# Kernel tuning notes

Hardware: AMD Instinct MI355X
Metric: run time of the kernel (lower is better)

## Reference

```python
import jax, jax.numpy as jnp
import numpy as np

B, C, N = 64, 512, 512  # batch, channels (=in_dim), last dim (=in_dim)
OUT = 512
GROUPS = 32
EPS = 1e-5


def setup_inputs() -> dict:
    key = jax.random.key(0)
    ks = jax.random.split(key, 7)
    s = 1.0 / np.sqrt(C)
    return {
        "x": jax.random.normal(ks[0], (B, C, N), dtype=jnp.float32),
        "q_w": jax.random.normal(ks[1], (OUT, C), dtype=jnp.float32) * s,
        "q_b": jax.random.normal(ks[2], (OUT,), dtype=jnp.float32) * s,
        "k_w": jax.random.normal(ks[3], (OUT, C), dtype=jnp.float32) * s,
        "k_b": jax.random.normal(ks[4], (OUT,), dtype=jnp.float32) * s,
        "v_w": jax.random.normal(ks[5], (OUT, C), dtype=jnp.float32) * s,
        "v_b": jax.random.normal(ks[6], (OUT,), dtype=jnp.float32) * s,
        "gn_w": jnp.ones((C,), dtype=jnp.float32),
        "gn_b": jnp.zeros((C,), dtype=jnp.float32),
    }


def group_norm(x, w, b):
    # x: (B, C, N); 32 groups over channel dim, affine per-channel.
    Bb, Cc, Nn = x.shape
    xg = x.reshape(Bb, GROUPS, -1)
    mean = jnp.mean(xg, axis=-1, keepdims=True)
    var = jnp.var(xg, axis=-1, keepdims=True)
    xn = ((xg - mean) * jax.lax.rsqrt(var + EPS)).reshape(Bb, Cc, Nn)
    return xn * w[None, :, None] + b[None, :, None]


def reference(x, q_w, q_b, k_w, k_b, v_w, v_b, gn_w, gn_b):
    xn = group_norm(x, gn_w, gn_b)  # (B, C, N)
    # nn.Linear applies to the last dim (N == in_dim)
    q = jnp.einsum("bcn,dn->bcd", xn, q_w) + q_b  # (B, C, OUT)
    k = jnp.einsum("bcn,dn->bcd", xn, k_w) + k_b
    v = jnp.einsum("bcn,dn->bcd", xn, v_w) + v_b
    scale = 1.0 / jnp.sqrt(jnp.float32(OUT))
    scores = jnp.einsum("bqd,bkd->bqk", q, k) * scale  # (B, C, C)
    attn = jax.nn.softmax(scores, axis=-1)
    return jnp.einsum("bqk,bkd->bqd", attn, v)  # (B, C, OUT)
```

## Files before the change

### kernel.cpp

```cpp
#include <hip/hip_runtime.h>
#include <cstdint>

#define EPSV 1e-5f
#define SM_SCALE 0.044194173824159216f

typedef unsigned short u16;
typedef __attribute__((ext_vector_type(8))) short short8;
typedef __attribute__((ext_vector_type(4))) float f32x4;

__device__ __forceinline__ u16 f2bf(float f) {
  union { float f; uint32_t u; } v; v.f = f;
  return (u16)((v.u + 0x7FFFu + ((v.u >> 16) & 1u)) >> 16);
}

__device__ __forceinline__ float bf2f(u16 h) {
  union { uint32_t u; float f; } v; v.u = ((uint32_t)h) << 16; return v.f;
}

__device__ __forceinline__ void gload_lds16(const void* g, void* l) {
  __builtin_amdgcn_global_load_lds((const __attribute__((address_space(1))) void*)g,
                                   (__attribute__((address_space(3))) void*)l, 16, 0, 0);
}

__device__ __forceinline__ f32x4 mfma16(short8 a, short8 b, f32x4 c) {
  return __builtin_amdgcn_mfma_f32_16x16x32_bf16(a, b, c, 0, 0, 0);
}

__global__ __launch_bounds__(256) void gn_fused_k(const float* __restrict__ x,
                                                  const float* __restrict__ gw,
                                                  const float* __restrict__ gb,
                                                  u16* __restrict__ xn) {
  __shared__ float xs[8192];
  __shared__ float ls[4], lss[4];
  const int bg = blockIdx.x;
  const int g = bg & 31;
  const float* p = x + (size_t)bg * 8192;
  float s = 0.f, ss = 0.f;
#pragma unroll
  for (int i = 0; i < 8; ++i) {
    const int idx = i * 1024 + threadIdx.x * 4;
    float4 v = *reinterpret_cast<const float4*>(p + idx);
    *reinterpret_cast<float4*>(xs + idx) = v;
    s += v.x + v.y + v.z + v.w;
    ss += v.x * v.x + v.y * v.y + v.z * v.z + v.w * v.w;
  }
  for (int off = 32; off; off >>= 1) { s += __shfl_xor(s, off); ss += __shfl_xor(ss, off); }
  const int w = threadIdx.x >> 6;
  if ((threadIdx.x & 63) == 0) { ls[w] = s; lss[w] = ss; }
  __syncthreads();
  s = ls[0] + ls[1] + ls[2] + ls[3];
  ss = lss[0] + lss[1] + lss[2] + lss[3];
  const float inv_n = 1.0f / 8192.f;
  const float mean = s * inv_n;
  const float rstd = rsqrtf(ss * inv_n - mean * mean + EPSV);
#pragma unroll
  for (int j = 0; j < 4; ++j) {
    const int idx = j * 2048 + threadIdx.x * 8;
    const int c = g * 16 + (idx >> 9);
    const float sc = gw[c] * rstd;
    const float sh = gb[c] - mean * sc;
    u16 o[8];
#pragma unroll
    for (int e = 0; e < 8; ++e) o[e] = f2bf(xs[idx + e] * sc + sh);
    *reinterpret_cast<uint4*>(xn + (size_t)bg * 8192 + idx) = *reinterpret_cast<const uint4*>(o);
  }
}

__global__ __launch_bounds__(256) void cast3_k(const float* __restrict__ a,
                                               const float* __restrict__ b2,
                                               const float* __restrict__ c,
                                               u16* __restrict__ oa, u16* __restrict__ ob,
                                               u16* __restrict__ oc) {
  const int which = blockIdx.x >> 7;
  const float* in = which == 0 ? a : (which == 1 ? b2 : c);
  u16* out = which == 0 ? oa : (which == 1 ? ob : oc);
  size_t base = (((size_t)(blockIdx.x & 127)) * 256 + threadIdx.x) * 8;
  float4 v0 = *reinterpret_cast<const float4*>(in + base);
  float4 v1 = *reinterpret_cast<const float4*>(in + base + 4);
  u16 o[8];
  o[0] = f2bf(v0.x); o[1] = f2bf(v0.y); o[2] = f2bf(v0.z); o[3] = f2bf(v0.w);
  o[4] = f2bf(v1.x); o[5] = f2bf(v1.y); o[6] = f2bf(v1.z); o[7] = f2bf(v1.w);
  *reinterpret_cast<uint4*>(out + base) = *reinterpret_cast<const uint4*>(o);
}

template <int OUT_MODE>
__global__ __launch_bounds__(512, 1) void gemm256_k(const u16* __restrict__ A, size_t sA,
                                                    const u16* __restrict__ Bm, size_t sB,
                                                    const float* __restrict__ bias,
                                                    void* __restrict__ out, size_t sO) {
  __shared__ u16 smem[65536];
  const int d = blockIdx.x;
  const int wgid = (d & 7) * 32 + (d >> 3);
  const int b = wgid >> 2;
  const int tile = wgid & 3;
  const int tm = (tile >> 1) * 256, tn = (tile & 1) * 256;
  const u16* Ab = A + (size_t)b * sA;
  const u16* Bb = Bm + (size_t)b * sB;
  const int tid = threadIdx.x, w = tid >> 6, lane = tid & 63;
  const int rh = w >> 2, cw = w & 3;
  const int frow = lane & 15, cc = lane >> 4;
  f32x4 acc[8][4] = {};
  short8 af[8], bfr[2];

#define STAGEH(Lofs, Gp)                                                       \
  {                                                                            \
    const u16* gsrc_ = (Gp);                                                   \
    _Pragma("unroll")                                                          \
    for (int p_ = 0; p_ < 2; ++p_) {                                           \
      const int row_ = p_ * 64 + (tid >> 3);                                   \
      const int slot_ = (tid & 7) ^ (row_ & 7);                                \
      gload_lds16(gsrc_ + (size_t)row_ * 512 + slot_ * 8,                      \
                  &smem[(Lofs) + p_ * 4096 + tid * 8]);                        \
    }                                                                          \
  }

#define PHASE(VMN, QB, KS, CP, ...)                                            \
  {                                                                            \
    asm volatile("s_waitcnt vmcnt(" #VMN ")" ::: "memory");                    \
    __builtin_amdgcn_s_barrier();                                              \
    asm volatile("" ::: "memory");                                             \
    _Pragma("unroll")                                                          \
    for (int j_ = 0; j_ < 2; ++j_) {                                           \
      const int lrb_ = (cw & 1) * 64 + (CP) * 32 + j_ * 16 + frow;             \
      bfr[j_] = *reinterpret_cast<const short8*>(                              \
          &smem[(QB) + 16384 + (cw >> 1) * 8192 + lrb_ * 64 +                  \
                (((KS) * 4 + cc) ^ (lrb_ & 7)) * 8]);                          \
    }                                                                          \
    if ((CP) == 0) {                                                           \
      _Pragma("unroll")                                                        \
      for (int ri_ = 0; ri_ < 8; ++ri_) {                                      \
        const int lra_ = ri_ * 16 + frow;                                      \
        af[ri_] = *reinterpret_cast<const short8*>(                            \
            &smem[(QB) + rh * 8192 + lra_ * 64 +                               \
                  (((KS) * 4 + cc) ^ (lra_ & 7)) * 8]);                        \
      }                                                                        \
    }                                                                          \
    __VA_ARGS__                                                                \
    __builtin_amdgcn_s_setprio(1);                                             \
    _Pragma("unroll")                                                          \
    for (int ri_ = 0; ri_ < 8; ++ri_) {                                        \
      acc[ri_][(CP) * 2]     = mfma16(af[ri_], bfr[0], acc[ri_][(CP) * 2]);    \
      acc[ri_][(CP) * 2 + 1] = mfma16(af[ri_], bfr[1], acc[ri_][(CP) * 2 + 1]);\
    }                                                                          \
    __builtin_amdgcn_s_setprio(0);                                             \
    __builtin_amdgcn_s_barrier();                                              \
    asm volatile("" ::: "memory");                                             \
  }

  STAGEH(0,     Ab + (size_t)tm * 512);
  STAGEH(8192,  Ab + (size_t)(tm + 128) * 512);
  STAGEH(16384, Bb + (size_t)tn * 512);
  STAGEH(24576, Bb + (size_t)(tn + 128) * 512);
  STAGEH(32768, Ab + (size_t)tm * 512 + 64);

  for (int i = 0; i < 3; ++i) {
    const int k0c1 = i * 128 + 64;
    const int k0n2 = i * 128 + 128;
    const int k0n3 = i * 128 + 192;
    PHASE(2, 0, 0, 0,
          STAGEH(40960, Ab + (size_t)(tm + 128) * 512 + k0c1);
          STAGEH(49152, Bb + (size_t)tn * 512 + k0c1);)
    PHASE(6, 0, 0, 1,
          STAGEH(57344, Bb + (size_t)(tn + 128) * 512 + k0c1);)
    PHASE(6, 0, 1, 0, )
    PHASE(2, 0, 1, 1,
          STAGEH(0, Ab + (size_t)tm * 512 + k0n2);)
    PHASE(2, 32768, 0, 0,
          STAGEH(8192,  Ab + (size_t)(tm + 128) * 512 + k0n2);
          STAGEH(16384, Bb + (size_t)tn * 512 + k0n2);)
    PHASE(6, 32768, 0, 1,
          STAGEH(24576, Bb + (size_t)(tn + 128) * 512 + k0n2);)
    PHASE(6, 32768, 1, 0, )
    PHASE(2, 32768, 1, 1,
          STAGEH(32768, Ab + (size_t)tm * 512 + k0n3);)
  }
  PHASE(2, 0, 0, 0,
        STAGEH(40960, Ab + (size_t)(tm + 128) * 512 + 448);
        STAGEH(49152, Bb + (size_t)tn * 512 + 448);)
  PHASE(6, 0, 0, 1,
        STAGEH(57344, Bb + (size_t)(tn + 128) * 512 + 448);)
  PHASE(6, 0, 1, 0, )
  PHASE(2, 0, 1, 1, )
  PHASE(0, 32768, 0, 0, )
  PHASE(0, 32768, 0, 1, )
  PHASE(0, 32768, 1, 0, )
  PHASE(0, 32768, 1, 1, )
#undef PHASE
#undef STAGEH

  const int col0 = lane & 15, row0 = (lane >> 4) * 4;
#pragma unroll
  for (int ri = 0; ri < 8; ++ri) {
#pragma unroll
    for (int cj = 0; cj < 4; ++cj) {
      const int gc = tn + cw * 64 + cj * 16 + col0;
      const float bv = (OUT_MODE == 0) ? bias[gc] : 0.f;
#pragma unroll
      for (int r = 0; r < 4; ++r) {
        const int gr = tm + rh * 128 + ri * 16 + row0 + r;
        float v = acc[ri][cj][r];
        if (OUT_MODE == 0) v += bv;
        if (OUT_MODE == 1) v += bias[gr];
        if (OUT_MODE == 2)
          ((float*)out)[(size_t)b * sO + (size_t)gr * 512 + gc] = v;
        else
          ((u16*)out)[(size_t)b * sO + (size_t)gr * 512 + gc] = f2bf(v);
      }
    }
  }
}

__global__ __launch_bounds__(256) void rowsm_k(u16* __restrict__ S) {
  const int w = threadIdx.x >> 6, lane = threadIdx.x & 63;
  const size_t rbase = (size_t)blockIdx.x * 64 + (size_t)w * 16;
#pragma unroll 4
  for (int r = 0; r < 16; ++r) {
    u16* row = S + (rbase + r) * 512 + lane * 8;
    short8 v = *reinterpret_cast<const short8*>(row);
    float f[8];
#pragma unroll
    for (int e = 0; e < 8; ++e) f[e] = bf2f((u16)v[e]) * SM_SCALE;
    float m = f[0];
#pragma unroll
    for (int e = 1; e < 8; ++e) m = fmaxf(m, f[e]);
    for (int off = 32; off; off >>= 1) m = fmaxf(m, __shfl_xor(m, off));
    float s = 0.f;
#pragma unroll
    for (int e = 0; e < 8; ++e) { f[e] = __expf(f[e] - m); s += f[e]; }
    for (int off = 32; off; off >>= 1) s += __shfl_xor(s, off);
    const float inv = 1.0f / s;
    u16 o[8];
#pragma unroll
    for (int e = 0; e < 8; ++e) o[e] = f2bf(f[e] * inv);
    *reinterpret_cast<uint4*>(row) = *reinterpret_cast<const uint4*>(o);
  }
}

extern "C" void kernel_launch(void* const* d_in, const int* in_sizes, int n_in,
                              void* d_out, int out_size, void* d_ws, size_t ws_size,
                              hipStream_t stream) {
  const float* x = (const float*)d_in[0];
  const float* qw = (const float*)d_in[1];
  const float* qb = (const float*)d_in[2];
  const float* kw = (const float*)d_in[3];
  const float* kb = (const float*)d_in[4];
  const float* vw = (const float*)d_in[5];
  const float* vb = (const float*)d_in[6];
  const float* gnw = (const float*)d_in[7];
  const float* gnb = (const float*)d_in[8];

  char* ws = (char*)d_ws;
  u16* qwb = (u16*)(ws);
  u16* kwb = (u16*)(ws + 524288);
  u16* vwb = (u16*)(ws + 2 * 524288);
  u16* xn = (u16*)(ws + 4 * 524288);
  u16* Qb = xn + 16777216;
  u16* Kb = Qb + 16777216;
  u16* VT = Kb + 16777216;
  u16* S = xn;
  float* out = (float*)d_out;

  gn_fused_k<<<dim3(2048), dim3(256), 0, stream>>>(x, gnw, gnb, xn);
  cast3_k<<<dim3(384), dim3(256), 0, stream>>>(qw, kw, vw, qwb, kwb, vwb);
  gemm256_k<0><<<dim3(256), dim3(512), 0, stream>>>(xn, (size_t)262144, qwb, (size_t)0, qb, (void*)Qb, (size_t)262144);
  gemm256_k<0><<<dim3(256), dim3(512), 0, stream>>>(xn, (size_t)262144, kwb, (size_t)0, kb, (void*)Kb, (size_t)262144);
  gemm256_k<1><<<dim3(256), dim3(512), 0, stream>>>(vwb, (size_t)0, xn, (size_t)262144, vb, (void*)VT, (size_t)262144);
  gemm256_k<3><<<dim3(256), dim3(512), 0, stream>>>(Qb, (size_t)262144, Kb, (size_t)262144, (const float*)nullptr, (void*)S, (size_t)262144);
  rowsm_k<<<dim3(512), dim3(256), 0, stream>>>(S);
  gemm256_k<2><<<dim3(256), dim3(512), 0, stream>>>(S, (size_t)262144, VT, (size_t)262144, (const float*)nullptr, (void*)out, (size_t)262144);
}
```

Before: 149.8 us.

## Fuse softmax into attention GEMM epilogues and merge groupnorm with weight casts

Removes the standalone row-softmax kernel. The QK^T GEMM epilogue now writes exp(score*scale) directly, without subtracting the row max. The PV GEMM computes row sums with an extra MFMA against a vector of ones and divides by them in its epilogue. The weight-cast kernel is also folded into the groupnorm kernel as extra blocks, saving a launch and a full read and write of the score matrix. Skipping the max subtraction risks exp overflow if scores are large, and the extra row-sum MFMAs add some compute to the final GEMM.

```diff
diff --git a/kernel.cpp b/kernel.cpp
--- a/kernel.cpp
+++ b/kernel.cpp
@@ -13,10 +13,6 @@
   return (u16)((v.u + 0x7FFFu + ((v.u >> 16) & 1u)) >> 16);
 }
 
-__device__ __forceinline__ float bf2f(u16 h) {
-  union { uint32_t u; float f; } v; v.u = ((uint32_t)h) << 16; return v.f;
-}
-
 __device__ __forceinline__ void gload_lds16(const void* g, void* l) {
   __builtin_amdgcn_global_load_lds((const __attribute__((address_space(1))) void*)g,
                                    (__attribute__((address_space(3))) void*)l, 16, 0, 0);
@@ -26,10 +22,30 @@
   return __builtin_amdgcn_mfma_f32_16x16x32_bf16(a, b, c, 0, 0, 0);
 }
 
-__global__ __launch_bounds__(256) void gn_fused_k(const float* __restrict__ x,
-                                                  const float* __restrict__ gw,
-                                                  const float* __restrict__ gb,
-                                                  u16* __restrict__ xn) {
+__global__ __launch_bounds__(256) void gncast_k(const float* __restrict__ x,
+                                                const float* __restrict__ gw,
+                                                const float* __restrict__ gb,
+                                                u16* __restrict__ xn,
+                                                const float* __restrict__ qw,
+                                                const float* __restrict__ kw,
+                                                const float* __restrict__ vw,
+                                                u16* __restrict__ qwb,
+                                                u16* __restrict__ kwb,
+                                                u16* __restrict__ vwb) {
+  if (blockIdx.x >= 2048) {
+    const int cb = blockIdx.x - 2048;
+    const int which = cb >> 7;
+    const float* in = which == 0 ? qw : (which == 1 ? kw : vw);
+    u16* out = which == 0 ? qwb : (which == 1 ? kwb : vwb);
+    size_t base = (((size_t)(cb & 127)) * 256 + threadIdx.x) * 8;
+    float4 v0 = *reinterpret_cast<const float4*>(in + base);
+    float4 v1 = *reinterpret_cast<const float4*>(in + base + 4);
+    u16 o[8];
+    o[0] = f2bf(v0.x); o[1] = f2bf(v0.y); o[2] = f2bf(v0.z); o[3] = f2bf(v0.w);
+    o[4] = f2bf(v1.x); o[5] = f2bf(v1.y); o[6] = f2bf(v1.z); o[7] = f2bf(v1.w);
+    *reinterpret_cast<uint4*>(out + base) = *reinterpret_cast<const uint4*>(o);
+    return;
+  }
   __shared__ float xs[8192];
   __shared__ float ls[4], lss[4];
   const int bg = blockIdx.x;
@@ -64,23 +80,6 @@
     for (int e = 0; e < 8; ++e) o[e] = f2bf(xs[idx + e] * sc + sh);
     *reinterpret_cast<uint4*>(xn + (size_t)bg * 8192 + idx) = *reinterpret_cast<const uint4*>(o);
   }
-}
-
-__global__ __launch_bounds__(256) void cast3_k(const float* __restrict__ a,
-                                               const float* __restrict__ b2,
-                                               const float* __restrict__ c,
-                                               u16* __restrict__ oa, u16* __restrict__ ob,
-                                               u16* __restrict__ oc) {
-  const int which = blockIdx.x >> 7;
-  const float* in = which == 0 ? a : (which == 1 ? b2 : c);
-  u16* out = which == 0 ? oa : (which == 1 ? ob : oc);
-  size_t base = (((size_t)(blockIdx.x & 127)) * 256 + threadIdx.x) * 8;
-  float4 v0 = *reinterpret_cast<const float4*>(in + base);
-  float4 v1 = *reinterpret_cast<const float4*>(in + base + 4);
-  u16 o[8];
-  o[0] = f2bf(v0.x); o[1] = f2bf(v0.y); o[2] = f2bf(v0.z); o[3] = f2bf(v0.w);
-  o[4] = f2bf(v1.x); o[5] = f2bf(v1.y); o[6] = f2bf(v1.z); o[7] = f2bf(v1.w);
-  *reinterpret_cast<uint4*>(out + base) = *reinterpret_cast<const uint4*>(o);
 }
 
 template <int OUT_MODE>
@@ -100,6 +99,10 @@
   const int rh = w >> 2, cw = w & 3;
   const int frow = lane & 15, cc = lane >> 4;
   f32x4 acc[8][4] = {};
+  f32x4 rs[8] = {};
+  short8 ones8;
+#pragma unroll
+  for (int e = 0; e < 8; ++e) ones8[e] = (short)0x3F80;
   short8 af[8], bfr[2];
 
 #define STAGEH(Lofs, Gp)                                                       \
@@ -141,6 +144,11 @@
     for (int ri_ = 0; ri_ < 8; ++ri_) {                                        \
       acc[ri_][(CP) * 2]     = mfma16(af[ri_], bfr[0], acc[ri_][(CP) * 2]);    \
       acc[ri_][(CP) * 2 + 1] = mfma16(af[ri_], bfr[1], acc[ri_][(CP) * 2 + 1]);\
+    }                                                                          \
+    if (OUT_MODE == 5 && (CP) == 0) {                                          \
+      _Pragma("unroll")                                                        \
+      for (int ri_ = 0; ri_ < 8; ++ri_)                                        \
+        rs[ri_] = mfma16(af[ri_], ones8, rs[ri_]);                             \
     }                                                                          \
     __builtin_amdgcn_s_setprio(0);                                             \
     __builtin_amdgcn_s_barrier();                                              \
@@ -191,6 +199,11 @@
   const int col0 = lane & 15, row0 = (lane >> 4) * 4;
 #pragma unroll
   for (int ri = 0; ri < 8; ++ri) {
+    f32x4 inv;
+    if (OUT_MODE == 5) {
+#pragma unroll
+      for (int r = 0; r < 4; ++r) inv[r] = 1.0f / rs[ri][r];
+    }
 #pragma unroll
     for (int cj = 0; cj < 4; ++cj) {
       const int gc = tn + cw * 64 + cj * 16 + col0;
@@ -201,38 +214,16 @@
         float v = acc[ri][cj][r];
         if (OUT_MODE == 0) v += bv;
         if (OUT_MODE == 1) v += bias[gr];
-        if (OUT_MODE == 2)
-          ((float*)out)[(size_t)b * sO + (size_t)gr * 512 + gc] = v;
-        else
+        if (OUT_MODE == 5) {
+          ((float*)out)[(size_t)b * sO + (size_t)gr * 512 + gc] = v * inv[r];
+        } else if (OUT_MODE == 4) {
+          ((u16*)out)[(size_t)b * sO + (size_t)gr * 512 + gc] =
+              f2bf(__expf(v * SM_SCALE));
+        } else {
           ((u16*)out)[(size_t)b * sO + (size_t)gr * 512 + gc] = f2bf(v);
+        }
       }
     }
-  }
-}
-
-__global__ __launch_bounds__(256) void rowsm_k(u16* __restrict__ S) {
-  const int w = threadIdx.x >> 6, lane = threadIdx.x & 63;
-  const size_t rbase = (size_t)blockIdx.x * 64 + (size_t)w * 16;
-#pragma unroll 4
-  for (int r = 0; r < 16; ++r) {
-    u16* row = S + (rbase + r) * 512 + lane * 8;
-    short8 v = *reinterpret_cast<const short8*>(row);
-    float f[8];
-#pragma unroll
-    for (int e = 0; e < 8; ++e) f[e] = bf2f((u16)v[e]) * SM_SCALE;
-    float m = f[0];
-#pragma unroll
-    for (int e = 1; e < 8; ++e) m = fmaxf(m, f[e]);
-    for (int off = 32; off; off >>= 1) m = fmaxf(m, __shfl_xor(m, off));
-    float s = 0.f;
-#pragma unroll
-    for (int e = 0; e < 8; ++e) { f[e] = __expf(f[e] - m); s += f[e]; }
-    for (int off = 32; off; off >>= 1) s += __shfl_xor(s, off);
-    const float inv = 1.0f / s;
-    u16 o[8];
-#pragma unroll
-    for (int e = 0; e < 8; ++e) o[e] = f2bf(f[e] * inv);
-    *reinterpret_cast<uint4*>(row) = *reinterpret_cast<const uint4*>(o);
   }
 }
 
@@ -257,15 +248,13 @@
   u16* Qb = xn + 16777216;
   u16* Kb = Qb + 16777216;
   u16* VT = Kb + 16777216;
-  u16* S = xn;
+  u16* E = xn;
   float* out = (float*)d_out;
 
-  gn_fused_k<<<dim3(2048), dim3(256), 0, stream>>>(x, gnw, gnb, xn);
-  cast3_k<<<dim3(384), dim3(256), 0, stream>>>(qw, kw, vw, qwb, kwb, vwb);
+  gncast_k<<<dim3(2432), dim3(256), 0, stream>>>(x, gnw, gnb, xn, qw, kw, vw, qwb, kwb, vwb);
   gemm256_k<0><<<dim3(256), dim3(512), 0, stream>>>(xn, (size_t)262144, qwb, (size_t)0, qb, (void*)Qb, (size_t)262144);
   gemm256_k<0><<<dim3(256), dim3(512), 0, stream>>>(xn, (size_t)262144, kwb, (size_t)0, kb, (void*)Kb, (size_t)262144);
   gemm256_k<1><<<dim3(256), dim3(512), 0, stream>>>(vwb, (size_t)0, xn, (size_t)262144, vb, (void*)VT, (size_t)262144);
-  gemm256_k<3><<<dim3(256), dim3(512), 0, stream>>>(Qb, (size_t)262144, Kb, (size_t)262144, (const float*)nullptr, (void*)S, (size_t)262144);
-  rowsm_k<<<dim3(512), dim3(256), 0, stream>>>(S);
-  gemm256_k<2><<<dim3(256), dim3(512), 0, stream>>>(S, (size_t)262144, VT, (size_t)262144, (const float*)nullptr, (void*)out, (size_t)262144);
-}
+  gemm256_k<4><<<dim3(256), dim3(512), 0, stream>>>(Qb, (size_t)262144, Kb, (size_t)262144, (const float*)nullptr, (void*)E, (size_t)262144);
+  gemm256_k<5><<<dim3(256), dim3(512), 0, stream>>>(E, (size_t)262144, VT, (size_t)262144, (const float*)nullptr, (void*)out, (size_t)262144);
+}
```

Result: faster. 139.3 us (-7.0%).
